# Optimization experiments

Measured on AMD Instinct MI355X. Metric: run time of the kernel, lower is better.

## Reference

```python
import jax, jax.numpy as jnp
import numpy as np

BETA = 0.5
ITERS = 20


def bjorck_orthonormalize(w, beta, iters):
    def body(w, _):
        wtw = jnp.matmul(w.T, w)            # [in, in]
        w = (1.0 + beta) * w - beta * jnp.matmul(w, wtw)
        return w, None
    w, _ = jax.lax.scan(body, w, None, length=iters)
    return w


def setup_inputs() -> dict:
    key = jax.random.key(0)
    k1, k2, k3 = jax.random.split(key, 3)
    x = jax.random.normal(k1, (4, 8192, 1024), dtype=jnp.float32)
    kernel = jax.random.normal(k2, (1024, 1024), dtype=jnp.float32)
    bias = jax.random.normal(k3, (1024,), dtype=jnp.float32)
    return {"x": x, "kernel": kernel, "bias": bias}


def reference(x, kernel, bias):
    # safe Bjorck scaling: sqrt(in_features * out_features)
    scaling = jnp.sqrt(jnp.asarray(kernel.shape[0] * kernel.shape[1], dtype=kernel.dtype))
    w = bjorck_orthonormalize(kernel / scaling, BETA, ITERS)  # [in, out]
    y = jnp.einsum('bsi,io->bso', x, w)
    y = y + bias.reshape((1, 1, -1))
    return y
```

## Files before the change

### kernel.cpp

```cpp
#include <hip/hip_runtime.h>
#include <cstdint>

typedef _Float16 half8 __attribute__((ext_vector_type(8)));
typedef _Float16 half4v __attribute__((ext_vector_type(4)));
typedef float f32x4 __attribute__((ext_vector_type(4)));

__device__ __forceinline__ void async_copy16(const void* g, void* l) {
    __builtin_amdgcn_global_load_lds((const __attribute__((address_space(1))) void*)g,
                                     (__attribute__((address_space(3))) void*)l, 16, 0, 0);
}

__global__ __launch_bounds__(256) void prep_w(const float* __restrict__ K,
                                              _Float16* __restrict__ w0,
                                              _Float16* __restrict__ w0T) {
    __shared__ float tile[64][65];
    const int t  = threadIdx.x;
    const int bi = blockIdx.y * 64;
    const int bj = blockIdx.x * 64;
    const int r0 = t >> 4;
    const int c4 = (t & 15) * 4;
#pragma unroll
    for (int rr = 0; rr < 4; ++rr) {
        int r = r0 + rr * 16;
        f32x4 v = *(const f32x4*)&K[(size_t)(bi + r) * 1024 + bj + c4];
        v *= 0.03125f;
        half4v h;
        h[0] = (_Float16)v[0]; h[1] = (_Float16)v[1];
        h[2] = (_Float16)v[2]; h[3] = (_Float16)v[3];
        *(half4v*)&w0[(size_t)(bi + r) * 1024 + bj + c4] = h;
        tile[r][c4 + 0] = v[0]; tile[r][c4 + 1] = v[1];
        tile[r][c4 + 2] = v[2]; tile[r][c4 + 3] = v[3];
    }
    __syncthreads();
    const int cT = t >> 4;
    const int rT = (t & 15) * 4;
#pragma unroll
    for (int cc = 0; cc < 4; ++cc) {
        int c = cT + cc * 16;
        half4v h;
        h[0] = (_Float16)tile[rT + 0][c]; h[1] = (_Float16)tile[rT + 1][c];
        h[2] = (_Float16)tile[rT + 2][c]; h[3] = (_Float16)tile[rT + 3][c];
        *(half4v*)&w0T[(size_t)(bj + c) * 1024 + bi + rT] = h;
    }
}

template <int EPI>
__global__ __launch_bounds__(512) void gemm1k(const _Float16* __restrict__ A,
                                              const _Float16* __restrict__ BT,
                                              const _Float16* __restrict__ wcur,
                                              _Float16* __restrict__ out,
                                              _Float16* __restrict__ outT) {
    __shared__ _Float16 sA[2][8192];
    __shared__ _Float16 sB[2][8192];
    const int t = threadIdx.x;
    const int b = blockIdx.x;
    const int xcd = b & 7, j = b >> 3;
    const int m0 = (((xcd & 1) << 3) + (j & 7)) << 6;
    const int n0 = (((xcd >> 1) << 2) + (j >> 3)) << 6;
    const int ln = t & 63, wv = t >> 6;
    const int wm = wv >> 1, wn = wv & 1;
    const int q  = ln >> 4, l15 = ln & 15;

    f32x4 acc[2];
#pragma unroll
    for (int jn = 0; jn < 2; ++jn) {
        acc[jn][0] = 0.f; acc[jn][1] = 0.f;
        acc[jn][2] = 0.f; acc[jn][3] = 0.f;
    }

    auto stage = [&](int buf, int k0) {
#pragma unroll
        for (int rnd = 0; rnd < 2; ++rnd) {
            int c = t + rnd * 512;
            int row = c >> 4, g = c & 15;
            int gs = g ^ (row & 15);
            async_copy16(A + (size_t)(m0 + row) * 1024 + k0 + gs * 8, &sA[buf][c * 8]);
            async_copy16(BT + (size_t)(n0 + row) * 1024 + k0 + gs * 8, &sB[buf][c * 8]);
        }
    };
    auto frag = [&](const _Float16* s, int row, int kc) -> half8 {
        return *(const half8*)&s[row * 128 + ((kc ^ (row & 15)) << 3)];
    };

    stage(0, 0);
    int cur = 0;
#pragma unroll 1
    for (int it = 0; it < 8; ++it) {
        __syncthreads();
        if (it < 7) stage(cur ^ 1, (it + 1) * 128);
#pragma unroll
        for (int kk = 0; kk < 4; ++kk) {
            half8 a0 = frag(sA[cur], wm * 16 + l15, kk * 4 + q);
            half8 b0 = frag(sB[cur], wn * 32 + 0  + l15, kk * 4 + q);
            half8 b1 = frag(sB[cur], wn * 32 + 16 + l15, kk * 4 + q);
            acc[0] = __builtin_amdgcn_mfma_f32_16x16x32_f16(a0, b0, acc[0], 0, 0, 0);
            acc[1] = __builtin_amdgcn_mfma_f32_16x16x32_f16(a0, b1, acc[1], 0, 0, 0);
        }
        cur ^= 1;
    }

    const int row0 = m0 + wm * 16 + q * 4;
#pragma unroll
    for (int jn = 0; jn < 2; ++jn) {
        int col = n0 + wn * 32 + jn * 16 + l15;
        if (EPI == 0) {
#pragma unroll
            for (int r = 0; r < 4; ++r)
                out[(size_t)(row0 + r) * 1024 + col] = (_Float16)acc[jn][r];
        } else {
            half4v hT;
#pragma unroll
            for (int r = 0; r < 4; ++r) {
                float w0v = (float)wcur[(size_t)(row0 + r) * 1024 + col];
                float nv  = 1.5f * w0v - 4.8828125e-4f * acc[jn][r];
                _Float16 h = (_Float16)nv;
                out[(size_t)(row0 + r) * 1024 + col] = h;
                hT[r] = h;
            }
            *(half4v*)&outT[(size_t)col * 1024 + row0] = hT;
        }
    }
}

__global__ __launch_bounds__(256) void gemm_big(const float* __restrict__ X,
                                                const _Float16* __restrict__ BT,
                                                const float* __restrict__ bias,
                                                float* __restrict__ Y) {
    __shared__ _Float16 sA[2][128 * 40];
    __shared__ _Float16 sB[2][128 * 32];
    const int t  = threadIdx.x;
    const int m0 = blockIdx.x * 128, n0 = blockIdx.y * 128;
    const int ln = t & 63, wv = t >> 6;
    const int wm = wv >> 1, wn = wv & 1;
    const int q  = ln >> 4, l15 = ln & 15;

    f32x4 acc[4][4];
#pragma unroll
    for (int i = 0; i < 4; ++i)
#pragma unroll
        for (int j = 0; j < 4; ++j) {
            acc[i][j][0] = 0.f; acc[i][j][1] = 0.f;
            acc[i][j][2] = 0.f; acc[i][j][3] = 0.f;
        }

    auto loadA = [&](int k0, f32x4* va) {
#pragma unroll
        for (int rnd = 0; rnd < 4; ++rnd) {
            int c = t + rnd * 256;
            int row = c >> 3, s4 = c & 7;
            va[rnd] = *(const f32x4*)&X[(size_t)(m0 + row) * 1024 + k0 + s4 * 4];
        }
    };
    auto writeA = [&](int buf, const f32x4* va) {
#pragma unroll
        for (int rnd = 0; rnd < 4; ++rnd) {
            int c = t + rnd * 256;
            int row = c >> 3, s4 = c & 7;
            half4v h;
            h[0] = (_Float16)va[rnd][0]; h[1] = (_Float16)va[rnd][1];
            h[2] = (_Float16)va[rnd][2]; h[3] = (_Float16)va[rnd][3];
            *(half4v*)&sA[buf][row * 40 + s4 * 4] = h;
        }
    };
    auto stageB = [&](int buf, int k0) {
#pragma unroll
        for (int rnd = 0; rnd < 2; ++rnd) {
            int c = t + rnd * 256;
            int row = c >> 2, s = c & 3;
            int gs = s ^ ((row >> 1) & 3);
            async_copy16(BT + (size_t)(n0 + row) * 1024 + k0 + gs * 8, &sB[buf][c * 8]);
        }
    };

    f32x4 va[4];
    loadA(0, va);
    stageB(0, 0);
    writeA(0, va);
    int cur = 0;
#pragma unroll 1
    for (int it = 0; it < 32; ++it) {
        __syncthreads();
        if (it < 31) {
            loadA((it + 1) * 32, va);
            stageB(cur ^ 1, (it + 1) * 32);
        }
        half8 a[4], b[4];
#pragma unroll
        for (int im = 0; im < 4; ++im) {
            int row = wm * 64 + im * 16 + l15;
            a[im] = *(const half8*)&sA[cur][row * 40 + q * 8];
        }
#pragma unroll
        for (int jn = 0; jn < 4; ++jn) {
            int row = wn * 64 + jn * 16 + l15;
            b[jn] = *(const half8*)&sB[cur][row * 32 + ((q ^ ((row >> 1) & 3)) << 3)];
        }
#pragma unroll
        for (int im = 0; im < 4; ++im)
#pragma unroll
            for (int jn = 0; jn < 4; ++jn)
                acc[im][jn] = __builtin_amdgcn_mfma_f32_16x16x32_f16(a[im], b[jn], acc[im][jn], 0, 0, 0);
        if (it < 31) writeA(cur ^ 1, va);
        cur ^= 1;
    }

#pragma unroll
    for (int jn = 0; jn < 4; ++jn) {
        int col = n0 + wn * 64 + jn * 16 + l15;
        float bv = bias[col];
#pragma unroll
        for (int im = 0; im < 4; ++im) {
            int row0 = m0 + wm * 64 + im * 16 + q * 4;
#pragma unroll
            for (int r = 0; r < 4; ++r)
                Y[(size_t)(row0 + r) * 1024 + col] = acc[im][jn][r] * 0.03125f + bv;
        }
    }
}

extern "C" void kernel_launch(void* const* d_in, const int* in_sizes, int n_in,
                              void* d_out, int out_size, void* d_ws, size_t ws_size,
                              hipStream_t stream) {
    (void)in_sizes; (void)n_in; (void)out_size; (void)ws_size;
    const float* x    = (const float*)d_in[0];
    const float* kern = (const float*)d_in[1];
    const float* bias = (const float*)d_in[2];
    float* y = (float*)d_out;

    char* ws = (char*)d_ws;
    const size_t SZ = (size_t)1024 * 1024 * sizeof(_Float16);
    _Float16* wh[2] = {(_Float16*)(ws + 0 * SZ), (_Float16*)(ws + 1 * SZ)};
    _Float16* wT[2] = {(_Float16*)(ws + 2 * SZ), (_Float16*)(ws + 3 * SZ)};
    _Float16* Sh    = (_Float16*)(ws + 4 * SZ);

    prep_w<<<dim3(16, 16), 256, 0, stream>>>(kern, wh[0], wT[0]);

    for (int it = 0; it < 20; ++it) {
        int c = it & 1, n = c ^ 1;
        gemm1k<0><<<256, 512, 0, stream>>>(wT[c], wT[c], nullptr, Sh, nullptr);
        gemm1k<1><<<256, 512, 0, stream>>>(wh[c], Sh, wh[c], wh[n], wT[n]);
    }
    gemm_big<<<dim3(256, 8), 256, 0, stream>>>(x, wT[0], bias, y);
}
```

Before: 756.8 us.

## Fuse Bjorck iterations into one persistent kernel with grid barriers

Replaces the 40 separate small GEMM launches of the Bjorck iteration with a single persistent 256-block kernel that synchronises between GEMMs using an atomic-counter grid barrier, reset by the prep kernel. This removes per-launch overhead and tail gaps between dependent small GEMMs. The big GEMM also gets an XCD-aware block-to-tile mapping for L2 locality and nontemporal output stores. The barrier assumes all 256 blocks are co-resident, otherwise it can deadlock.

```diff
diff --git a/kernel.cpp b/kernel.cpp
--- a/kernel.cpp
+++ b/kernel.cpp
@@ -12,7 +12,9 @@
 
 __global__ __launch_bounds__(256) void prep_w(const float* __restrict__ K,
                                               _Float16* __restrict__ w0,
-                                              _Float16* __restrict__ w0T) {
+                                              _Float16* __restrict__ w0T,
+                                              unsigned* __restrict__ cnt) {
+    if (blockIdx.x == 0 && blockIdx.y == 0 && threadIdx.x == 0) *cnt = 0u;
     __shared__ float tile[64][65];
     const int t  = threadIdx.x;
     const int bi = blockIdx.y * 64;
@@ -44,12 +46,10 @@
     }
 }
 
-template <int EPI>
-__global__ __launch_bounds__(512) void gemm1k(const _Float16* __restrict__ A,
-                                              const _Float16* __restrict__ BT,
-                                              const _Float16* __restrict__ wcur,
-                                              _Float16* __restrict__ out,
-                                              _Float16* __restrict__ outT) {
+__global__ __launch_bounds__(512)
+void bjorck_chain(_Float16* __restrict__ wh0, _Float16* __restrict__ wh1,
+                  _Float16* __restrict__ wT0, _Float16* __restrict__ wT1,
+                  _Float16* __restrict__ Sh,  unsigned* __restrict__ cnt) {
     __shared__ _Float16 sA[2][8192];
     __shared__ _Float16 sB[2][8192];
     const int t = threadIdx.x;
@@ -61,64 +61,94 @@
     const int wm = wv >> 1, wn = wv & 1;
     const int q  = ln >> 4, l15 = ln & 15;
 
-    f32x4 acc[2];
-#pragma unroll
-    for (int jn = 0; jn < 2; ++jn) {
-        acc[jn][0] = 0.f; acc[jn][1] = 0.f;
-        acc[jn][2] = 0.f; acc[jn][3] = 0.f;
-    }
-
-    auto stage = [&](int buf, int k0) {
-#pragma unroll
-        for (int rnd = 0; rnd < 2; ++rnd) {
-            int c = t + rnd * 512;
-            int row = c >> 4, g = c & 15;
-            int gs = g ^ (row & 15);
-            async_copy16(A + (size_t)(m0 + row) * 1024 + k0 + gs * 8, &sA[buf][c * 8]);
-            async_copy16(BT + (size_t)(n0 + row) * 1024 + k0 + gs * 8, &sB[buf][c * 8]);
-        }
-    };
-    auto frag = [&](const _Float16* s, int row, int kc) -> half8 {
-        return *(const half8*)&s[row * 128 + ((kc ^ (row & 15)) << 3)];
-    };
-
-    stage(0, 0);
-    int cur = 0;
+    unsigned phase = 0;
+
+    auto gbar = [&]() {
+        __syncthreads();
+        ++phase;
+        if (t == 0) {
+            __hip_atomic_fetch_add(cnt, 1u, __ATOMIC_RELEASE, __HIP_MEMORY_SCOPE_AGENT);
+            const unsigned tgt = phase * 256u;
+            while (__hip_atomic_load(cnt, __ATOMIC_RELAXED, __HIP_MEMORY_SCOPE_AGENT) < tgt)
+                __builtin_amdgcn_s_sleep(1);
+            __threadfence();
+        }
+        __syncthreads();
+    };
+
+    auto run_gemm = [&](const _Float16* __restrict__ A, const _Float16* __restrict__ BT,
+                        const _Float16* __restrict__ wcur, _Float16* __restrict__ out,
+                        _Float16* __restrict__ outT, int EPI) {
+        f32x4 acc[2];
+#pragma unroll
+        for (int jn = 0; jn < 2; ++jn) {
+            acc[jn][0] = 0.f; acc[jn][1] = 0.f;
+            acc[jn][2] = 0.f; acc[jn][3] = 0.f;
+        }
+        auto stage = [&](int buf, int k0) {
+#pragma unroll
+            for (int rnd = 0; rnd < 2; ++rnd) {
+                int c = t + rnd * 512;
+                int row = c >> 4, g = c & 15;
+                int gs = g ^ (row & 15);
+                async_copy16(A + (size_t)(m0 + row) * 1024 + k0 + gs * 8, &sA[buf][c * 8]);
+                async_copy16(BT + (size_t)(n0 + row) * 1024 + k0 + gs * 8, &sB[buf][c * 8]);
+            }
+        };
+        auto frag = [&](const _Float16* s, int row, int kc) -> half8 {
+            return *(const half8*)&s[row * 128 + ((kc ^ (row & 15)) << 3)];
+        };
+
+        stage(0, 0);
+        int cur = 0;
 #pragma unroll 1
-    for (int it = 0; it < 8; ++it) {
-        __syncthreads();
-        if (it < 7) stage(cur ^ 1, (it + 1) * 128);
-#pragma unroll
-        for (int kk = 0; kk < 4; ++kk) {
-            half8 a0 = frag(sA[cur], wm * 16 + l15, kk * 4 + q);
-            half8 b0 = frag(sB[cur], wn * 32 + 0  + l15, kk * 4 + q);
-            half8 b1 = frag(sB[cur], wn * 32 + 16 + l15, kk * 4 + q);
-            acc[0] = __builtin_amdgcn_mfma_f32_16x16x32_f16(a0, b0, acc[0], 0, 0, 0);
-            acc[1] = __builtin_amdgcn_mfma_f32_16x16x32_f16(a0, b1, acc[1], 0, 0, 0);
-        }
-        cur ^= 1;
-    }
-
-    const int row0 = m0 + wm * 16 + q * 4;
-#pragma unroll
-    for (int jn = 0; jn < 2; ++jn) {
-        int col = n0 + wn * 32 + jn * 16 + l15;
-        if (EPI == 0) {
-#pragma unroll
-            for (int r = 0; r < 4; ++r)
-                out[(size_t)(row0 + r) * 1024 + col] = (_Float16)acc[jn][r];
-        } else {
-            half4v hT;
-#pragma unroll
-            for (int r = 0; r < 4; ++r) {
-                float w0v = (float)wcur[(size_t)(row0 + r) * 1024 + col];
-                float nv  = 1.5f * w0v - 4.8828125e-4f * acc[jn][r];
-                _Float16 h = (_Float16)nv;
-                out[(size_t)(row0 + r) * 1024 + col] = h;
-                hT[r] = h;
+        for (int it8 = 0; it8 < 8; ++it8) {
+            __syncthreads();
+            if (it8 < 7) stage(cur ^ 1, (it8 + 1) * 128);
+#pragma unroll
+            for (int kk = 0; kk < 4; ++kk) {
+                half8 a0 = frag(sA[cur], wm * 16 + l15, kk * 4 + q);
+                half8 b0 = frag(sB[cur], wn * 32 + 0  + l15, kk * 4 + q);
+                half8 b1 = frag(sB[cur], wn * 32 + 16 + l15, kk * 4 + q);
+                acc[0] = __builtin_amdgcn_mfma_f32_16x16x32_f16(a0, b0, acc[0], 0, 0, 0);
+                acc[1] = __builtin_amdgcn_mfma_f32_16x16x32_f16(a0, b1, acc[1], 0, 0, 0);
             }
-            *(half4v*)&outT[(size_t)col * 1024 + row0] = hT;
-        }
+            cur ^= 1;
+        }
+
+        const int row0 = m0 + wm * 16 + q * 4;
+#pragma unroll
+        for (int jn = 0; jn < 2; ++jn) {
+            int col = n0 + wn * 32 + jn * 16 + l15;
+            if (EPI == 0) {
+#pragma unroll
+                for (int r = 0; r < 4; ++r)
+                    out[(size_t)(row0 + r) * 1024 + col] = (_Float16)acc[jn][r];
+            } else {
+                half4v hT;
+#pragma unroll
+                for (int r = 0; r < 4; ++r) {
+                    float w0v = (float)wcur[(size_t)(row0 + r) * 1024 + col];
+                    float nv  = 1.5f * w0v - 4.8828125e-4f * acc[jn][r];
+                    _Float16 h = (_Float16)nv;
+                    out[(size_t)(row0 + r) * 1024 + col] = h;
+                    hT[r] = h;
+                }
+                *(half4v*)&outT[(size_t)col * 1024 + row0] = hT;
+            }
+        }
+    };
+
+#pragma unroll 1
+    for (int it = 0; it < 20; ++it) {
+        _Float16* whc = (it & 1) ? wh1 : wh0;
+        _Float16* whn = (it & 1) ? wh0 : wh1;
+        _Float16* wTc = (it & 1) ? wT1 : wT0;
+        _Float16* wTn = (it & 1) ? wT0 : wT1;
+        run_gemm(wTc, wTc, nullptr, Sh, nullptr, 0);
+        gbar();
+        run_gemm(whc, Sh, whc, whn, wTn, 1);
+        gbar();
     }
 }
 
@@ -128,8 +158,15 @@
                                                 float* __restrict__ Y) {
     __shared__ _Float16 sA[2][128 * 40];
     __shared__ _Float16 sB[2][128 * 32];
-    const int t  = threadIdx.x;
-    const int m0 = blockIdx.x * 128, n0 = blockIdx.y * 128;
+    const int t   = threadIdx.x;
+    const int bb  = blockIdx.x;
+    const int xcd = bb & 7;
+    const int jj  = bb >> 3;
+    const int rr  = jj >> 5;
+    const int ss  = jj & 31;
+    const int mt  = rr * 32 + xcd * 4 + (ss >> 3);
+    const int nt  = ss & 7;
+    const int m0 = mt * 128, n0 = nt * 128;
     const int ln = t & 63, wv = t >> 6;
     const int wm = wv >> 1, wn = wv & 1;
     const int q  = ln >> 4, l15 = ln & 15;
@@ -184,7 +221,7 @@
             loadA((it + 1) * 32, va);
             stageB(cur ^ 1, (it + 1) * 32);
         }
-        half8 a[4], b[4];
+        half8 a[4], bfr[4];
 #pragma unroll
         for (int im = 0; im < 4; ++im) {
             int row = wm * 64 + im * 16 + l15;
@@ -193,13 +230,13 @@
 #pragma unroll
         for (int jn = 0; jn < 4; ++jn) {
             int row = wn * 64 + jn * 16 + l15;
-            b[jn] = *(const half8*)&sB[cur][row * 32 + ((q ^ ((row >> 1) & 3)) << 3)];
+            bfr[jn] = *(const half8*)&sB[cur][row * 32 + ((q ^ ((row >> 1) & 3)) << 3)];
         }
 #pragma unroll
         for (int im = 0; im < 4; ++im)
 #pragma unroll
             for (int jn = 0; jn < 4; ++jn)
-                acc[im][jn] = __builtin_amdgcn_mfma_f32_16x16x32_f16(a[im], b[jn], acc[im][jn], 0, 0, 0);
+                acc[im][jn] = __builtin_amdgcn_mfma_f32_16x16x32_f16(a[im], bfr[jn], acc[im][jn], 0, 0, 0);
         if (it < 31) writeA(cur ^ 1, va);
         cur ^= 1;
     }
@@ -213,7 +250,8 @@
             int row0 = m0 + wm * 64 + im * 16 + q * 4;
 #pragma unroll
             for (int r = 0; r < 4; ++r)
-                Y[(size_t)(row0 + r) * 1024 + col] = acc[im][jn][r] * 0.03125f + bv;
+                __builtin_nontemporal_store(acc[im][jn][r] * 0.03125f + bv,
+                                            &Y[(size_t)(row0 + r) * 1024 + col]);
         }
     }
 }
@@ -232,13 +270,11 @@
     _Float16* wh[2] = {(_Float16*)(ws + 0 * SZ), (_Float16*)(ws + 1 * SZ)};
     _Float16* wT[2] = {(_Float16*)(ws + 2 * SZ), (_Float16*)(ws + 3 * SZ)};
     _Float16* Sh    = (_Float16*)(ws + 4 * SZ);
-
-    prep_w<<<dim3(16, 16), 256, 0, stream>>>(kern, wh[0], wT[0]);
-
-    for (int it = 0; it < 20; ++it) {
-        int c = it & 1, n = c ^ 1;
-        gemm1k<0><<<256, 512, 0, stream>>>(wT[c], wT[c], nullptr, Sh, nullptr);
-        gemm1k<1><<<256, 512, 0, stream>>>(wh[c], Sh, wh[c], wh[n], wT[n]);
-    }
-    gemm_big<<<dim3(256, 8), 256, 0, stream>>>(x, wT[0], bias, y);
-}
+    unsigned* cnt   = (unsigned*)(ws + 5 * SZ);
+
+    prep_w<<<dim3(16, 16), 256, 0, stream>>>(kern, wh[0], wT[0], cnt);
+
+    bjorck_chain<<<256, 512, 0, stream>>>(wh[0], wh[1], wT[0], wT[1], Sh, cnt);
+
+    gemm_big<<<2048, 256, 0, stream>>>(x, wT[0], bias, y);
+}
```

Result: slower. 1.552 ms (+105.1%).
